# Optimization experiments

Measured on AMD Instinct MI355X. Metric: run time of the kernel, lower is better.

The kernel has to match this reference:

```python
import jax, jax.numpy as jnp
import numpy as np

N, D, K, NUM_CLASSES = 65536, 512, 1024, 2


def setup_inputs() -> dict:
    key = jax.random.key(0)
    kx, kc = jax.random.split(key)
    x = jax.random.normal(kx, (N, D), dtype=jnp.float32)
    codebook_vectors = jax.random.normal(kc, (K, D), dtype=jnp.float32)
    codebook_classes = jnp.arange(K, dtype=jnp.int64 if jax.config.read('jax_enable_x64') else jnp.int32) % NUM_CLASSES
    return {"x": x, "codebook_vectors": codebook_vectors, "codebook_classes": codebook_classes}


def reference(x, codebook_vectors, codebook_classes):
    # Squared Euclidean distances (argmin identical to torch.cdist's p=2 argmin):
    # d2[n,k] = |x_n|^2 - 2 x_n . c_k + |c_k|^2
    x_sq = jnp.sum(x * x, axis=1, keepdims=True)            # (N, 1)
    c_sq = jnp.sum(codebook_vectors * codebook_vectors, axis=1)  # (K,)
    cross = jnp.einsum('nd,kd->nk', x, codebook_vectors)    # (N, K) GEMM
    d2 = x_sq - 2.0 * cross + c_sq[None, :]
    winners = jnp.argmin(d2, axis=1)                         # (N,)
    return codebook_classes[winners]
```

## Files before the change

### kernel.cpp

```cpp
#include <hip/hip_runtime.h>
#include <hip/hip_bf16.h>


#define N_ROWS 65536
#define DIM    512
#define K_CB   1024
#define NT     16
#define LDSBUF_F 16384
#define LDSBUF   32768

typedef short bf16x8 __attribute__((ext_vector_type(8)));
typedef float f32x4  __attribute__((ext_vector_type(4)));
typedef unsigned short u16x8 __attribute__((ext_vector_type(8)));

__device__ __forceinline__ unsigned short f2bf_rn(float f) {
    unsigned u = __float_as_uint(f);
    unsigned r = (u + 0x7FFFu + ((u >> 16) & 1u)) >> 16;
    return (unsigned short)r;
}
__device__ __forceinline__ float bf2f(unsigned short h) {
    return __uint_as_float(((unsigned)h) << 16);
}

__device__ __forceinline__ void gload16(const void* g, void* l) {
    __builtin_amdgcn_global_load_lds(
        (const __attribute__((address_space(1))) unsigned int*)g,
        (__attribute__((address_space(3))) unsigned int*)l, 16, 0, 0);
}

__global__ void csq_kernel(const float* __restrict__ C, float* __restrict__ csq) {
    int wid  = (blockIdx.x * blockDim.x + threadIdx.x) >> 6;
    int lane = threadIdx.x & 63;
    const float4* p = (const float4*)(C + (size_t)wid * DIM);
    float4 a = p[lane * 2];
    float4 b = p[lane * 2 + 1];
    float s = a.x*a.x + a.y*a.y + a.z*a.z + a.w*a.w
            + b.x*b.x + b.y*b.y + b.z*b.z + b.w*b.w;
    #pragma unroll
    for (int m = 1; m < 64; m <<= 1) s += __shfl_xor(s, m, 64);
    if (lane == 0) csq[wid] = s;
}

__global__ void split_hi8(const float* __restrict__ src,
                          unsigned short* __restrict__ h, int n8) {
    int stride = gridDim.x * 256;
    for (int i = blockIdx.x * 256 + threadIdx.x; i < n8; i += stride) {
        const float4* p = (const float4*)(src + (size_t)i * 8);
        float4 a = p[0], b = p[1];
        u16x8 o;
        o[0] = f2bf_rn(a.x); o[1] = f2bf_rn(a.y);
        o[2] = f2bf_rn(a.z); o[3] = f2bf_rn(a.w);
        o[4] = f2bf_rn(b.x); o[5] = f2bf_rn(b.y);
        o[6] = f2bf_rn(b.z); o[7] = f2bf_rn(b.w);
        *(u16x8*)(h + (size_t)i * 8) = o;
    }
}

__global__ __launch_bounds__(512, 2)
void gemm_scores(const unsigned short* __restrict__ Xh,
                 const unsigned short* __restrict__ Ch,
                 const float* __restrict__ csq,
                 _Float16* __restrict__ scores) {
    extern __shared__ unsigned short smem[];

    int b  = blockIdx.x;
    int x  = b & 7;
    int m8 = b >> 3;
    int rowtile = x * 32 + (m8 >> 2);
    int coltile = m8 & 3;
    int n0 = rowtile * 256;
    int k0 = coltile * 256;

    int tid  = threadIdx.x;
    int w    = tid >> 6;
    int lane = tid & 63;
    int wr   = w >> 2, wc = w & 3;
    int rbase = wr * 128, cbase = wc * 64;
    int lrow = lane & 15;
    int lk   = lane >> 4;
    int sg   = lk ^ ((lrow >> 1) & 3);

    int srow = tid >> 2;
    int sgrp = tid & 3;
    int r1   = (srow < 64) ? srow : srow + 64;
    int ggA  = sgrp ^ ((r1 >> 1) & 3);
    int gB   = sgrp ^ ((srow >> 1) & 3);
    size_t oA1 = (size_t)(n0 + r1) * DIM + ggA * 8;
    size_t oA2 = oA1 + (size_t)64 * DIM;
    size_t oB0 = (size_t)(k0 + srow) * DIM + gB * 8;
    size_t oB1 = oB0 + (size_t)128 * DIM;
    int rowA1_0 = (w < 4) ? w * 16 : w * 16 + 64;
    int dA1  = rowA1_0 * 32;
    int dA2  = dA1 + 2048;
    int dB0  = 8192 + w * 512;
    int dB1  = dB0 + 4096;

    f32x4 acc[8][4];
    #pragma unroll
    for (int i = 0; i < 8; i++)
        #pragma unroll
        for (int j = 0; j < 4; j++)
            acc[i][j] = (f32x4){0.f, 0.f, 0.f, 0.f};

    auto issue_tile = [&](int t) {
        unsigned short* bufn = smem + (t & 1) * LDSBUF_F;
        size_t d = (size_t)t * 32;
        gload16(Xh + oA1 + d, bufn + dA1);
        gload16(Xh + oA2 + d, bufn + dA2);
        gload16(Ch + oB0 + d, bufn + dB0);
        gload16(Ch + oB1 + d, bufn + dB1);
    };

    issue_tile(0);

    for (int t = 0; t < NT; ++t) {
        asm volatile("s_waitcnt vmcnt(0)" ::: "memory");
        __builtin_amdgcn_s_barrier();
        asm volatile("" ::: "memory");

        const unsigned short* buf = smem + (t & 1) * LDSBUF_F;
        const unsigned short* pA = buf + (rbase + lrow) * 32 + sg * 8;
        const unsigned short* pB = buf + 8192 + (cbase + lrow) * 32 + sg * 8;

        bf16x8 bh[4], ah[8];
        #pragma unroll
        for (int n = 0; n < 4; n++) bh[n] = *(const bf16x8*)(pB + n * 512);
        #pragma unroll
        for (int m = 0; m < 8; m++) ah[m] = *(const bf16x8*)(pA + m * 512);
        if (t + 1 < NT) issue_tile(t + 1);

        __builtin_amdgcn_s_setprio(1);
        #pragma unroll
        for (int m = 0; m < 8; m++)
            #pragma unroll
            for (int n = 0; n < 4; n++)
                acc[m][n] = __builtin_amdgcn_mfma_f32_16x16x32_bf16(ah[m], bh[n], acc[m][n], 0, 0, 0);
        __builtin_amdgcn_s_setprio(0);
    }

    float cs[4];
    #pragma unroll
    for (int n = 0; n < 4; n++) cs[n] = csq[k0 + cbase + n * 16 + lrow];

    #pragma unroll
    for (int m = 0; m < 8; m++) {
        int grow = n0 + rbase + m * 16 + lk * 4;
        #pragma unroll
        for (int r = 0; r < 4; r++) {
            _Float16* sp = scores + (size_t)(grow + r) * K_CB + k0 + cbase + lrow;
            #pragma unroll
            for (int n = 0; n < 4; n++)
                sp[n * 16] = (_Float16)(cs[n] - 2.0f * acc[m][n][r]);
        }
    }
}

struct H8 { _Float16 v[8]; };

__global__ __launch_bounds__(256)
void phase2_kernel(const float* __restrict__ X, const float* __restrict__ C,
                   const float* __restrict__ csq,
                   const _Float16* __restrict__ scores,
                   const int* __restrict__ classes, int* __restrict__ out) {
    int lane = threadIdx.x & 63;
    int n = blockIdx.x * 4 + (threadIdx.x >> 6);

    float s[16];
    {
        const _Float16* sp16 = scores + (size_t)n * K_CB + lane * 16;
        H8 h0 = *(const H8*)sp16;
        H8 h1 = *(const H8*)(sp16 + 8);
        #pragma unroll
        for (int j = 0; j < 8; j++) {
            s[j]     = (float)h0.v[j];
            s[8 + j] = (float)h1.v[j];
        }
    }

    float mn = s[0];
    #pragma unroll
    for (int j = 1; j < 16; j++) mn = fminf(mn, s[j]);
    #pragma unroll
    for (int m = 1; m < 64; m <<= 1) mn = fminf(mn, __shfl_xor(mn, m, 64));

    float thr = mn + 16.0f;
    unsigned fl = 0;
    #pragma unroll
    for (int j = 0; j < 16; j++) fl |= (unsigned)(s[j] <= thr) << j;
    int cnt = __popc(fl);
    #pragma unroll
    for (int m = 1; m < 64; m <<= 1) cnt += __shfl_xor(cnt, m, 64);

    int bestk;
    if (cnt == 1) {
        int kk = 0x7fffffff;
        #pragma unroll
        for (int j = 0; j < 16; j++)
            if ((fl >> j) & 1) kk = lane * 16 + j;
        #pragma unroll
        for (int m = 1; m < 64; m <<= 1) kk = min(kk, __shfl_xor(kk, m, 64));
        bestk = kk;
    } else {
        const float4* xp = (const float4*)(X + (size_t)n * DIM + lane * 8);
        float4 x0 = xp[0], x1 = xp[1];
        float bv = 3.4e38f;
        int bk = 0x7fffffff;
        #pragma unroll 1
        for (int j = 0; j < 16; j++) {
            unsigned long long mask = __ballot((fl >> j) & 1);
            while (mask) {
                int l = __ffsll((unsigned long long)mask) - 1;
                mask &= mask - 1;
                int k = l * 16 + j;
                const float4* cp = (const float4*)(C + (size_t)k * DIM + lane * 8);
                float4 y0 = cp[0], y1 = cp[1];
                float d = x0.x*y0.x + x0.y*y0.y + x0.z*y0.z + x0.w*y0.w
                        + x1.x*y1.x + x1.y*y1.y + x1.z*y1.z + x1.w*y1.w;
                #pragma unroll
                for (int m = 1; m < 64; m <<= 1) d += __shfl_xor(d, m, 64);
                float se = csq[k] - 2.0f * d;
                if (se < bv || (se == bv && k < bk)) { bv = se; bk = k; }
            }
        }
        bestk = bk;
    }
    if (lane == 0) out[n] = classes[bestk];
}

__global__ void init_kernel(unsigned long long* __restrict__ packed) {
    int n = blockIdx.x * 256 + threadIdx.x;
    if (n < N_ROWS) packed[n] = ~0ull;
}

__global__ void split_kernel(const float* __restrict__ src,
                             unsigned short* __restrict__ h,
                             unsigned short* __restrict__ l, int n4) {
    int stride = gridDim.x * 256;
    for (int i = blockIdx.x * 256 + threadIdx.x; i < n4; i += stride) {
        float4 v = ((const float4*)src)[i];
        ushort4 hh, ll;
        float f;
        f = v.x; hh.x = f2bf_rn(f); ll.x = f2bf_rn(f - bf2f(hh.x));
        f = v.y; hh.y = f2bf_rn(f); ll.y = f2bf_rn(f - bf2f(hh.y));
        f = v.z; hh.z = f2bf_rn(f); ll.z = f2bf_rn(f - bf2f(hh.z));
        f = v.w; hh.w = f2bf_rn(f); ll.w = f2bf_rn(f - bf2f(hh.w));
        ((ushort4*)h)[i] = hh;
        ((ushort4*)l)[i] = ll;
    }
}

__global__ __launch_bounds__(512, 2)
void gemm_argmin(const unsigned short* __restrict__ Xh,
                 const unsigned short* __restrict__ Xl,
                 const unsigned short* __restrict__ Ch,
                 const unsigned short* __restrict__ Cl,
                 const float* __restrict__ csq,
                 unsigned long long* __restrict__ packed) {
    extern __shared__ unsigned short smem[];

    int b  = blockIdx.x;
    int x  = b & 7;
    int m8 = b >> 3;
    int rowtile = x * 32 + (m8 >> 2);
    int coltile = m8 & 3;
    int n0 = rowtile * 256;
    int k0 = coltile * 256;

    int tid  = threadIdx.x;
    int w    = tid >> 6;
    int lane = tid & 63;
    int wr   = w >> 2, wc = w & 3;
    int rbase = wr * 128, cbase = wc * 64;
    int lrow = lane & 15;
    int lk   = lane >> 4;
    int sg   = lk ^ ((lrow >> 1) & 3);

    int srow = tid >> 2;
    int sgrp = tid & 3;
    int r1   = (srow < 64) ? srow : srow + 64;
    int ggA  = sgrp ^ ((r1 >> 1) & 3);
    int gB   = sgrp ^ ((srow >> 1) & 3);
    size_t oA1 = (size_t)(n0 + r1) * DIM + ggA * 8;
    size_t oA2 = oA1 + (size_t)64 * DIM;
    size_t oB0 = (size_t)(k0 + srow) * DIM + gB * 8;
    size_t oB1 = oB0 + (size_t)128 * DIM;
    int rowA1_0 = (w < 4) ? w * 16 : w * 16 + 64;
    int dA1  = rowA1_0 * 32;
    int dA2  = dA1 + 2048;
    int dB0  = 16384 + w * 512;
    int dB1  = dB0 + 4096;
    int dBl0 = dB0 + 8192;
    int dBl1 = dB1 + 8192;

    f32x4 acc[8][4];
    #pragma unroll
    for (int i = 0; i < 8; i++)
        #pragma unroll
        for (int j = 0; j < 4; j++)
            acc[i][j] = (f32x4){0.f, 0.f, 0.f, 0.f};

    bf16x8 bh[4], bl[4];

    auto issue_tile = [&](int t) {
        unsigned short* bufn = smem + (t & 1) * LDSBUF;
        size_t d = (size_t)t * 32;
        gload16(Xh + oA1 + d, bufn + dA1);
        gload16(Xl + oA1 + d, bufn + 8192 + dA1);
        gload16(Ch + oB0 + d, bufn + dB0);
        gload16(Ch + oB1 + d, bufn + dB1);
        gload16(Cl + oB0 + d, bufn + dBl0);
        gload16(Cl + oB1 + d, bufn + dBl1);
        gload16(Xh + oA2 + d, bufn + dA2);
        gload16(Xl + oA2 + d, bufn + 8192 + dA2);
    };

    auto mfma_half = [&](int mb, const bf16x8* ah, const bf16x8* al) {
        __builtin_amdgcn_s_setprio(1);
        #pragma unroll
        for (int mm = 0; mm < 4; mm++)
            #pragma unroll
            for (int n = 0; n < 4; n++)
                acc[mb + mm][n] = __builtin_amdgcn_mfma_f32_16x16x32_bf16(ah[mm], bh[n], acc[mb + mm][n], 0, 0, 0);
        #pragma unroll
        for (int mm = 0; mm < 4; mm++)
            #pragma unroll
            for (int n = 0; n < 4; n++)
                acc[mb + mm][n] = __builtin_amdgcn_mfma_f32_16x16x32_bf16(ah[mm], bl[n], acc[mb + mm][n], 0, 0, 0);
        #pragma unroll
        for (int mm = 0; mm < 4; mm++)
            #pragma unroll
            for (int n = 0; n < 4; n++)
                acc[mb + mm][n] = __builtin_amdgcn_mfma_f32_16x16x32_bf16(al[mm], bh[n], acc[mb + mm][n], 0, 0, 0);
        __builtin_amdgcn_s_setprio(0);
    };

    issue_tile(0);

    for (int t = 0; t < NT; ++t) {
        asm volatile("s_waitcnt vmcnt(0)" ::: "memory");
        __builtin_amdgcn_s_barrier();
        asm volatile("" ::: "memory");

        const unsigned short* buf = smem + (t & 1) * LDSBUF;
        const unsigned short* pA = buf + (rbase + lrow) * 32 + sg * 8;
        const unsigned short* pB = buf + 16384 + (cbase + lrow) * 32 + sg * 8;

        #pragma unroll
        for (int n = 0; n < 4; n++) {
            bh[n] = *(const bf16x8*)(pB + n * 512);
            bl[n] = *(const bf16x8*)(pB + 8192 + n * 512);
        }
        bf16x8 ah[4], al[4];
        #pragma unroll
        for (int mm = 0; mm < 4; mm++) {
            ah[mm] = *(const bf16x8*)(pA + mm * 512);
            al[mm] = *(const bf16x8*)(pA + 8192 + mm * 512);
        }
        if (t + 1 < NT) issue_tile(t + 1);

        mfma_half(0, ah, al);

        bf16x8 ah2[4], al2[4];
        #pragma unroll
        for (int mm = 0; mm < 4; mm++) {
            ah2[mm] = *(const bf16x8*)(pA + (4 + mm) * 512);
            al2[mm] = *(const bf16x8*)(pA + 8192 + (4 + mm) * 512);
        }
        mfma_half(4, ah2, al2);
    }

    float cs[4];
    #pragma unroll
    for (int n = 0; n < 4; n++) cs[n] = csq[k0 + cbase + n * 16 + lrow];

    #pragma unroll
    for (int m = 0; m < 8; m++) {
        #pragma unroll
        for (int r = 0; r < 4; r++) {
            unsigned long long best = ~0ull;
            #pragma unroll
            for (int n = 0; n < 4; n++) {
                float s = cs[n] - 2.0f * acc[m][n][r];
                unsigned kb  = __float_as_uint(s);
                unsigned key = kb ^ (unsigned)(((int)kb >> 31) | 0x80000000);
                unsigned col = (unsigned)(k0 + cbase + n * 16 + lrow);
                unsigned long long pk = (((unsigned long long)key) << 32) | col;
                best = pk < best ? pk : best;
            }
            #pragma unroll
            for (int mask = 1; mask <= 8; mask <<= 1) {
                unsigned hi = __shfl_xor((unsigned)(best >> 32), mask, 64);
                unsigned lo = __shfl_xor((unsigned)(best & 0xFFFFFFFFu), mask, 64);
                unsigned long long other = (((unsigned long long)hi) << 32) | lo;
                best = other < best ? other : best;
            }
            if (lrow == 0) {
                int grow = n0 + rbase + m * 16 + lk * 4 + r;
                atomicMin(&packed[grow], best);
            }
        }
    }
}

__global__ void map_kernel(const unsigned long long* __restrict__ packed,
                           const int* __restrict__ classes,
                           int* __restrict__ out) {
    int n = blockIdx.x * 256 + threadIdx.x;
    if (n < N_ROWS) {
        unsigned col = (unsigned)(packed[n] & 0xFFFFFFFFull);
        out[n] = classes[col];
    }
}

extern "C" void kernel_launch(void* const* d_in, const int* in_sizes, int n_in,
                              void* d_out, int out_size, void* d_ws, size_t ws_size,
                              hipStream_t stream) {
    const float* X       = (const float*)d_in[0];
    const float* C       = (const float*)d_in[1];
    const int*   classes = (const int*)d_in[2];
    int*         out     = (int*)d_out;
    char* ws = (char*)d_ws;

    {
        size_t off = 0;
        float* csq = (float*)(ws + off);                  off += 4096;
        unsigned short* Xh = (unsigned short*)(ws + off); off += (size_t)N_ROWS * DIM * 2;
        unsigned short* Ch = (unsigned short*)(ws + off); off += (size_t)K_CB * DIM * 2;
        _Float16* scores = (_Float16*)(ws + off);         off += (size_t)N_ROWS * K_CB * 2;
        if (ws_size >= off) {
            csq_kernel<<<K_CB / 4, 256, 0, stream>>>(C, csq);
            split_hi8<<<2048, 256, 0, stream>>>(X, Xh, N_ROWS * DIM / 8);
            split_hi8<<<256, 256, 0, stream>>>(C, Ch, K_CB * DIM / 8);
            hipFuncSetAttribute((const void*)gemm_scores,
                                hipFuncAttributeMaxDynamicSharedMemorySize,
                                2 * LDSBUF_F * (int)sizeof(unsigned short));
            gemm_scores<<<(N_ROWS / 256) * (K_CB / 256), 512,
                          2 * LDSBUF_F * sizeof(unsigned short), stream>>>(
                Xh, Ch, csq, scores);
            phase2_kernel<<<N_ROWS / 4, 256, 0, stream>>>(X, C, csq, scores, classes, out);
            return;
        }
    }

    size_t off = 0;
    unsigned long long* packed = (unsigned long long*)(ws + off); off += (size_t)N_ROWS * 8;
    float* csq = (float*)(ws + off);                              off += (size_t)K_CB * 4;
    unsigned short* Xh = (unsigned short*)(ws + off);             off += (size_t)N_ROWS * DIM * 2;
    unsigned short* Xl = (unsigned short*)(ws + off);             off += (size_t)N_ROWS * DIM * 2;
    unsigned short* Ch = (unsigned short*)(ws + off);             off += (size_t)K_CB * DIM * 2;
    unsigned short* Cl = (unsigned short*)(ws + off);             off += (size_t)K_CB * DIM * 2;

    init_kernel<<<N_ROWS / 256, 256, 0, stream>>>(packed);
    csq_kernel<<<K_CB / 4, 256, 0, stream>>>(C, csq);
    split_kernel<<<2048, 256, 0, stream>>>(X, Xh, Xl, N_ROWS * DIM / 4);
    split_kernel<<<512, 256, 0, stream>>>(C, Ch, Cl, K_CB * DIM / 4);
    hipFuncSetAttribute((const void*)gemm_argmin,
                        hipFuncAttributeMaxDynamicSharedMemorySize,
                        2 * LDSBUF * (int)sizeof(unsigned short));
    gemm_argmin<<<(N_ROWS / 256) * (K_CB / 256), 512,
                  2 * LDSBUF * sizeof(unsigned short), stream>>>(
        Xh, Xl, Ch, Cl, csq, packed);
    map_kernel<<<N_ROWS / 256, 256, 0, stream>>>(packed, classes, out);
}
```

Measured before the change: 181.6 us.

## Fuse X fp32-to-bf16 conversion into GEMM A-tile loading

Drops the separate split_hi8 pass over X. The GEMM now loads fp32 X rows into registers two tiles ahead, converts them to bf16 and writes them into the swizzled LDS buffer after the MFMA block. This removes a full write and re-read of a bf16 copy of X. In exchange the fp32 A reads are twice as large, are repeated by each of the 4 column tiles, and add register pressure and hand-written vmcnt bookkeeping inside the main loop.

```diff
diff --git a/kernel.cpp b/kernel.cpp
--- a/kernel.cpp
+++ b/kernel.cpp
@@ -20,6 +20,14 @@
 }
 __device__ __forceinline__ float bf2f(unsigned short h) {
     return __uint_as_float(((unsigned)h) << 16);
+}
+__device__ __forceinline__ bf16x8 pack_bf8(float4 a, float4 b) {
+    bf16x8 r;
+    r[0] = (short)f2bf_rn(a.x); r[1] = (short)f2bf_rn(a.y);
+    r[2] = (short)f2bf_rn(a.z); r[3] = (short)f2bf_rn(a.w);
+    r[4] = (short)f2bf_rn(b.x); r[5] = (short)f2bf_rn(b.y);
+    r[6] = (short)f2bf_rn(b.z); r[7] = (short)f2bf_rn(b.w);
+    return r;
 }
 
 __device__ __forceinline__ void gload16(const void* g, void* l) {
@@ -57,7 +65,7 @@
 }
 
 __global__ __launch_bounds__(512, 2)
-void gemm_scores(const unsigned short* __restrict__ Xh,
+void gemm_scores(const float* __restrict__ X,
                  const unsigned short* __restrict__ Ch,
                  const float* __restrict__ csq,
                  _Float16* __restrict__ scores) {
@@ -80,18 +88,19 @@
     int lk   = lane >> 4;
     int sg   = lk ^ ((lrow >> 1) & 3);
 
+    int arow = tid >> 2;
+    int ag   = tid & 3;
+    int aswz = (arow >> 1) & 3;
+    const float* xsrc0 = X + (size_t)(n0 + arow) * DIM + ag * 8;
+    const float* xsrc1 = xsrc0 + (size_t)128 * DIM;
+    int adst0 = arow * 32 + (ag ^ aswz) * 8;
+    int adst1 = adst0 + 4096;
+
     int srow = tid >> 2;
     int sgrp = tid & 3;
-    int r1   = (srow < 64) ? srow : srow + 64;
-    int ggA  = sgrp ^ ((r1 >> 1) & 3);
     int gB   = sgrp ^ ((srow >> 1) & 3);
-    size_t oA1 = (size_t)(n0 + r1) * DIM + ggA * 8;
-    size_t oA2 = oA1 + (size_t)64 * DIM;
     size_t oB0 = (size_t)(k0 + srow) * DIM + gB * 8;
     size_t oB1 = oB0 + (size_t)128 * DIM;
-    int rowA1_0 = (w < 4) ? w * 16 : w * 16 + 64;
-    int dA1  = rowA1_0 * 32;
-    int dA2  = dA1 + 2048;
     int dB0  = 8192 + w * 512;
     int dB1  = dB0 + 4096;
 
@@ -102,19 +111,35 @@
         for (int j = 0; j < 4; j++)
             acc[i][j] = (f32x4){0.f, 0.f, 0.f, 0.f};
 
-    auto issue_tile = [&](int t) {
-        unsigned short* bufn = smem + (t & 1) * LDSBUF_F;
-        size_t d = (size_t)t * 32;
-        gload16(Xh + oA1 + d, bufn + dA1);
-        gload16(Xh + oA2 + d, bufn + dA2);
+    auto issue_B = [&](int tn) {
+        unsigned short* bufn = smem + (tn & 1) * LDSBUF_F;
+        size_t d = (size_t)tn * 32;
         gload16(Ch + oB0 + d, bufn + dB0);
         gload16(Ch + oB1 + d, bufn + dB1);
     };
 
-    issue_tile(0);
-
-    for (int t = 0; t < NT; ++t) {
-        asm volatile("s_waitcnt vmcnt(0)" ::: "memory");
+    float4 ga0, ga1, gb0, gb1, fa0, fa1, fb0, fb1;
+
+    {
+        const float4* p0 = (const float4*)xsrc0;
+        const float4* p1 = (const float4*)xsrc1;
+        ga0 = p0[0]; ga1 = p0[1]; gb0 = p1[0]; gb1 = p1[1];
+        issue_B(0);
+        const float4* q0 = (const float4*)(xsrc0 + 32);
+        const float4* q1 = (const float4*)(xsrc1 + 32);
+        fa0 = q0[0]; fa1 = q0[1]; fb0 = q1[0]; fb1 = q1[1];
+        asm volatile("s_waitcnt vmcnt(6)" ::: "memory");
+        unsigned short* b0 = smem;
+        *(bf16x8*)(b0 + adst0) = pack_bf8(ga0, ga1);
+        *(bf16x8*)(b0 + adst1) = pack_bf8(gb0, gb1);
+    }
+
+    auto body = [&](int t,
+                    float4& ua0, float4& ua1, float4& ub0, float4& ub1,
+                    float4& va0, float4& va1, float4& vb0, float4& vb1) {
+        if (t + 1 < NT) asm volatile("s_waitcnt vmcnt(4)" ::: "memory");
+        else            asm volatile("s_waitcnt vmcnt(0)" ::: "memory");
+        asm volatile("s_waitcnt lgkmcnt(0)" ::: "memory");
         __builtin_amdgcn_s_barrier();
         asm volatile("" ::: "memory");
 
@@ -127,7 +152,13 @@
         for (int n = 0; n < 4; n++) bh[n] = *(const bf16x8*)(pB + n * 512);
         #pragma unroll
         for (int m = 0; m < 8; m++) ah[m] = *(const bf16x8*)(pA + m * 512);
-        if (t + 1 < NT) issue_tile(t + 1);
+
+        if (t + 1 < NT) issue_B(t + 1);
+        if (t + 2 < NT) {
+            const float4* q0 = (const float4*)(xsrc0 + (t + 2) * 32);
+            const float4* q1 = (const float4*)(xsrc1 + (t + 2) * 32);
+            ua0 = q0[0]; ua1 = q0[1]; ub0 = q1[0]; ub1 = q1[1];
+        }
 
         __builtin_amdgcn_s_setprio(1);
         #pragma unroll
@@ -136,6 +167,19 @@
             for (int n = 0; n < 4; n++)
                 acc[m][n] = __builtin_amdgcn_mfma_f32_16x16x32_bf16(ah[m], bh[n], acc[m][n], 0, 0, 0);
         __builtin_amdgcn_s_setprio(0);
+
+        if (t + 1 < NT) {
+            if (t + 2 < NT) asm volatile("s_waitcnt vmcnt(6)" ::: "memory");
+            else            asm volatile("s_waitcnt vmcnt(2)" ::: "memory");
+            unsigned short* nb = smem + ((t + 1) & 1) * LDSBUF_F;
+            *(bf16x8*)(nb + adst0) = pack_bf8(va0, va1);
+            *(bf16x8*)(nb + adst1) = pack_bf8(vb0, vb1);
+        }
+    };
+
+    for (int tt = 0; tt < NT; tt += 2) {
+        body(tt,     ga0, ga1, gb0, gb1, fa0, fa1, fb0, fb1);
+        body(tt + 1, fa0, fa1, fb0, fb1, ga0, ga1, gb0, gb1);
     }
 
     float cs[4];
@@ -424,19 +468,17 @@
     {
         size_t off = 0;
         float* csq = (float*)(ws + off);                  off += 4096;
-        unsigned short* Xh = (unsigned short*)(ws + off); off += (size_t)N_ROWS * DIM * 2;
         unsigned short* Ch = (unsigned short*)(ws + off); off += (size_t)K_CB * DIM * 2;
         _Float16* scores = (_Float16*)(ws + off);         off += (size_t)N_ROWS * K_CB * 2;
         if (ws_size >= off) {
             csq_kernel<<<K_CB / 4, 256, 0, stream>>>(C, csq);
-            split_hi8<<<2048, 256, 0, stream>>>(X, Xh, N_ROWS * DIM / 8);
             split_hi8<<<256, 256, 0, stream>>>(C, Ch, K_CB * DIM / 8);
             hipFuncSetAttribute((const void*)gemm_scores,
                                 hipFuncAttributeMaxDynamicSharedMemorySize,
                                 2 * LDSBUF_F * (int)sizeof(unsigned short));
             gemm_scores<<<(N_ROWS / 256) * (K_CB / 256), 512,
                           2 * LDSBUF_F * sizeof(unsigned short), stream>>>(
-                Xh, Ch, csq, scores);
+                X, Ch, csq, scores);
             phase2_kernel<<<N_ROWS / 4, 256, 0, stream>>>(X, C, csq, scores, classes, out);
             return;
         }
```

Result: faster. 158.1 us (median of 3 runs) (-12.9%).

## Fuse X fp32-to-bf16 conversion into GEMM tile loads with 64-wide K tiles

Applied to the files above, without the earlier changes.

Removes the separate split_hi8 pass over X. The GEMM now loads fp32 X rows into registers, converts them to bf16 and writes them into swizzled LDS itself, while codebook tiles still arrive through direct global-to-LDS loads. The K tile doubles to 64 with a wider XOR swizzle, which halves the barriers, and LDS use doubles so occupancy drops to one block per CU. This saves one write and one read of the bf16 X array. In exchange the GEMM reads fp32 X, twice the bytes, and spends extra VALU work and registers on conversion inside the main loop.

```diff
diff --git a/kernel.cpp b/kernel.cpp
--- a/kernel.cpp
+++ b/kernel.cpp
@@ -5,9 +5,10 @@
 #define N_ROWS 65536
 #define DIM    512
 #define K_CB   1024
+#define NT2    8
+#define LDSB2  32768
+#define LDSBUF 32768
 #define NT     16
-#define LDSBUF_F 16384
-#define LDSBUF   32768
 
 typedef short bf16x8 __attribute__((ext_vector_type(8)));
 typedef float f32x4  __attribute__((ext_vector_type(4)));
@@ -20,6 +21,14 @@
 }
 __device__ __forceinline__ float bf2f(unsigned short h) {
     return __uint_as_float(((unsigned)h) << 16);
+}
+__device__ __forceinline__ bf16x8 pack_bf8(float4 a, float4 b) {
+    bf16x8 r;
+    r[0] = (short)f2bf_rn(a.x); r[1] = (short)f2bf_rn(a.y);
+    r[2] = (short)f2bf_rn(a.z); r[3] = (short)f2bf_rn(a.w);
+    r[4] = (short)f2bf_rn(b.x); r[5] = (short)f2bf_rn(b.y);
+    r[6] = (short)f2bf_rn(b.z); r[7] = (short)f2bf_rn(b.w);
+    return r;
 }
 
 __device__ __forceinline__ void gload16(const void* g, void* l) {
@@ -56,8 +65,8 @@
     }
 }
 
-__global__ __launch_bounds__(512, 2)
-void gemm_scores(const unsigned short* __restrict__ Xh,
+__global__ __launch_bounds__(512, 1)
+void gemm_scores(const float* __restrict__ X,
                  const unsigned short* __restrict__ Ch,
                  const float* __restrict__ csq,
                  _Float16* __restrict__ scores) {
@@ -78,22 +87,24 @@
     int rbase = wr * 128, cbase = wc * 64;
     int lrow = lane & 15;
     int lk   = lane >> 4;
-    int sg   = lk ^ ((lrow >> 1) & 3);
-
-    int srow = tid >> 2;
-    int sgrp = tid & 3;
-    int r1   = (srow < 64) ? srow : srow + 64;
-    int ggA  = sgrp ^ ((r1 >> 1) & 3);
-    int gB   = sgrp ^ ((srow >> 1) & 3);
-    size_t oA1 = (size_t)(n0 + r1) * DIM + ggA * 8;
-    size_t oA2 = oA1 + (size_t)64 * DIM;
-    size_t oB0 = (size_t)(k0 + srow) * DIM + gB * 8;
-    size_t oB1 = oB0 + (size_t)128 * DIM;
-    int rowA1_0 = (w < 4) ? w * 16 : w * 16 + 64;
-    int dA1  = rowA1_0 * 32;
-    int dA2  = dA1 + 2048;
-    int dB0  = 8192 + w * 512;
-    int dB1  = dB0 + 4096;
+    int swz  = (lrow >> 1) & 7;
+    int sgk0 = (lk)     ^ swz;
+    int sgk1 = (4 + lk) ^ swz;
+
+    int ra = tid >> 1;
+    int h  = tid & 1;
+    int aswz = (ra >> 1) & 7;
+    const float* xsrc = X + (size_t)(n0 + ra) * DIM + h * 32;
+    int ad0 = ra * 64 + ((h * 4 + 0) ^ aswz) * 8;
+    int ad1 = ra * 64 + ((h * 4 + 1) ^ aswz) * 8;
+    int ad2 = ra * 64 + ((h * 4 + 2) ^ aswz) * 8;
+    int ad3 = ra * 64 + ((h * 4 + 3) ^ aswz) * 8;
+
+    int rb  = tid >> 3;
+    int grp = tid & 7;
+    int gg  = grp ^ ((rb >> 1) & 7);
+    size_t oB = (size_t)(k0 + rb) * DIM + gg * 8;
+    int dB  = 16384 + w * 512;
 
     f32x4 acc[8][4];
     #pragma unroll
@@ -102,33 +113,56 @@
         for (int j = 0; j < 4; j++)
             acc[i][j] = (f32x4){0.f, 0.f, 0.f, 0.f};
 
-    auto issue_tile = [&](int t) {
-        unsigned short* bufn = smem + (t & 1) * LDSBUF_F;
-        size_t d = (size_t)t * 32;
-        gload16(Xh + oA1 + d, bufn + dA1);
-        gload16(Xh + oA2 + d, bufn + dA2);
-        gload16(Ch + oB0 + d, bufn + dB0);
-        gload16(Ch + oB1 + d, bufn + dB1);
+    auto issue_B = [&](int tn) {
+        unsigned short* bufn = smem + (tn & 1) * LDSB2;
+        size_t d = (size_t)tn * 64;
+        gload16(Ch + oB + d,                   bufn + dB);
+        gload16(Ch + oB + d + (size_t)64*DIM,  bufn + dB + 4096);
+        gload16(Ch + oB + d + (size_t)128*DIM, bufn + dB + 8192);
+        gload16(Ch + oB + d + (size_t)192*DIM, bufn + dB + 12288);
     };
 
-    issue_tile(0);
-
-    for (int t = 0; t < NT; ++t) {
+    float4 xq0, xq1, xq2, xq3, xq4, xq5, xq6, xq7;
+
+    auto loadX = [&](int tn) {
+        const float4* q = (const float4*)(xsrc + tn * 64);
+        xq0 = q[0]; xq1 = q[1]; xq2 = q[2]; xq3 = q[3];
+        xq4 = q[4]; xq5 = q[5]; xq6 = q[6]; xq7 = q[7];
+    };
+    auto writeA = [&](unsigned short* nb) {
+        *(bf16x8*)(nb + ad0) = pack_bf8(xq0, xq1);
+        *(bf16x8*)(nb + ad1) = pack_bf8(xq2, xq3);
+        *(bf16x8*)(nb + ad2) = pack_bf8(xq4, xq5);
+        *(bf16x8*)(nb + ad3) = pack_bf8(xq6, xq7);
+    };
+
+    loadX(0);
+    issue_B(0);
+    asm volatile("s_waitcnt vmcnt(4)" ::: "memory");
+    writeA(smem);
+
+    for (int t = 0; t < NT2; ++t) {
         asm volatile("s_waitcnt vmcnt(0)" ::: "memory");
+        asm volatile("s_waitcnt lgkmcnt(0)" ::: "memory");
         __builtin_amdgcn_s_barrier();
         asm volatile("" ::: "memory");
 
-        const unsigned short* buf = smem + (t & 1) * LDSBUF_F;
-        const unsigned short* pA = buf + (rbase + lrow) * 32 + sg * 8;
-        const unsigned short* pB = buf + 8192 + (cbase + lrow) * 32 + sg * 8;
-
-        bf16x8 bh[4], ah[8];
-        #pragma unroll
-        for (int n = 0; n < 4; n++) bh[n] = *(const bf16x8*)(pB + n * 512);
-        #pragma unroll
-        for (int m = 0; m < 8; m++) ah[m] = *(const bf16x8*)(pA + m * 512);
-        if (t + 1 < NT) issue_tile(t + 1);
-
+        const unsigned short* buf = smem + (t & 1) * LDSB2;
+        unsigned short* nbuf = smem + ((t + 1) & 1) * LDSB2;
+        const unsigned short* pA = buf + (rbase + lrow) * 64;
+        const unsigned short* pB = buf + 16384 + (cbase + lrow) * 64;
+        bool pre = (t + 1 < NT2);
+
+        if (pre) {
+            loadX(t + 1);
+            issue_B(t + 1);
+        }
+
+        bf16x8 ah[8], bh[4];
+        #pragma unroll
+        for (int n = 0; n < 4; n++) bh[n] = *(const bf16x8*)(pB + n * 1024 + sgk0 * 8);
+        #pragma unroll
+        for (int m = 0; m < 8; m++) ah[m] = *(const bf16x8*)(pA + m * 1024 + sgk0 * 8);
         __builtin_amdgcn_s_setprio(1);
         #pragma unroll
         for (int m = 0; m < 8; m++)
@@ -136,6 +170,22 @@
             for (int n = 0; n < 4; n++)
                 acc[m][n] = __builtin_amdgcn_mfma_f32_16x16x32_bf16(ah[m], bh[n], acc[m][n], 0, 0, 0);
         __builtin_amdgcn_s_setprio(0);
+        #pragma unroll
+        for (int n = 0; n < 4; n++) bh[n] = *(const bf16x8*)(pB + n * 1024 + sgk1 * 8);
+        #pragma unroll
+        for (int m = 0; m < 8; m++) ah[m] = *(const bf16x8*)(pA + m * 1024 + sgk1 * 8);
+        __builtin_amdgcn_s_setprio(1);
+        #pragma unroll
+        for (int m = 0; m < 8; m++)
+            #pragma unroll
+            for (int n = 0; n < 4; n++)
+                acc[m][n] = __builtin_amdgcn_mfma_f32_16x16x32_bf16(ah[m], bh[n], acc[m][n], 0, 0, 0);
+        __builtin_amdgcn_s_setprio(0);
+
+        if (pre) {
+            asm volatile("s_waitcnt vmcnt(4)" ::: "memory");
+            writeA(nbuf);
+        }
     }
 
     float cs[4];
@@ -424,19 +474,17 @@
     {
         size_t off = 0;
         float* csq = (float*)(ws + off);                  off += 4096;
-        unsigned short* Xh = (unsigned short*)(ws + off); off += (size_t)N_ROWS * DIM * 2;
         unsigned short* Ch = (unsigned short*)(ws + off); off += (size_t)K_CB * DIM * 2;
         _Float16* scores = (_Float16*)(ws + off);         off += (size_t)N_ROWS * K_CB * 2;
         if (ws_size >= off) {
             csq_kernel<<<K_CB / 4, 256, 0, stream>>>(C, csq);
-            split_hi8<<<2048, 256, 0, stream>>>(X, Xh, N_ROWS * DIM / 8);
             split_hi8<<<256, 256, 0, stream>>>(C, Ch, K_CB * DIM / 8);
             hipFuncSetAttribute((const void*)gemm_scores,
                                 hipFuncAttributeMaxDynamicSharedMemorySize,
-                                2 * LDSBUF_F * (int)sizeof(unsigned short));
+                                2 * LDSB2 * (int)sizeof(unsigned short));
             gemm_scores<<<(N_ROWS / 256) * (K_CB / 256), 512,
-                          2 * LDSBUF_F * sizeof(unsigned short), stream>>>(
-                Xh, Ch, csq, scores);
+                          2 * LDSB2 * sizeof(unsigned short), stream>>>(
+                X, Ch, csq, scores);
             phase2_kernel<<<N_ROWS / 4, 256, 0, stream>>>(X, C, csq, scores, classes, out);
             return;
         }
```

Result: slower. 194.3 us (+7.0%).
